# Performance work log

Measured on AMD Instinct MI355X. Metric: run time of the kernel, lower is better.

Reference implementation:

```python
import jax, jax.numpy as jnp
import numpy as np

BS, NCAMS, CIN, H, W = 4, 1, 256, 56, 200
MID = 128
DCH = 112  # (58-2)/0.5 depth bins
GX, GY, GZ = 128, 128, 16  # voxel grid


def setup_inputs() -> dict:
    key = jax.random.key(0)
    ks = jax.random.split(key, 32)
    f32 = jnp.float32

    def n(k, shape, scale=0.05):
        return jax.random.normal(k, shape, f32) * scale

    inp = {
        'img_feat': jax.random.normal(ks[0], (BS, NCAMS, CIN, H, W), f32),
        'scaled_pixel_size': jax.random.uniform(ks[1], (BS * NCAMS, 1), f32) * 2.0 + 0.5,
        # normalized sampling coords, slightly beyond [-1,1] to exercise zero padding
        'grids': jax.random.uniform(ks[2], (NCAMS, BS, GX, GY, GZ, 3), f32) * 2.2 - 1.1,
        # reduce_conv: Conv2d(CIN->MID,3x3,bias) + BN(affine, eval=per-channel scale/shift)
        'rc_w': n(ks[3], (MID, CIN, 3, 3)),
        'rc_b': n(ks[4], (MID,)),
        'rc_s': 1.0 + n(ks[5], (MID,)),
        'rc_t': n(ks[6], (MID,)),
        # Mlp(1 -> MID -> MID)
        'fc1_w': n(ks[7], (MID, 1), 0.5),
        'fc1_b': n(ks[8], (MID,)),
        'fc2_w': n(ks[9], (MID, MID)),
        'fc2_b': n(ks[10], (MID,)),
        # SELayer 1x1 convs (act on [N,MID,1,1] -> plain linears)
        'se_rw': n(ks[11], (MID, MID)),
        'se_rb': n(ks[12], (MID,)),
        'se_ew': n(ks[13], (MID, MID)),
        'se_eb': n(ks[14], (MID,)),
        # 3 BasicBlocks: conv3x3(no bias)+BN+ReLU+conv3x3(no bias)+BN, residual, ReLU
        'bb_w1': n(ks[15], (3, MID, MID, 3, 3)),
        'bb_s1': 1.0 + n(ks[16], (3, MID)),
        'bb_t1': n(ks[17], (3, MID)),
        'bb_w2': n(ks[18], (3, MID, MID, 3, 3)),
        'bb_s2': 1.0 + n(ks[19], (3, MID)),
        'bb_t2': n(ks[20], (3, MID)),
        # depth_pred 1x1 conv MID -> DCH
        'dp_w': n(ks[21], (DCH, MID)),
        'dp_b': n(ks[22], (DCH,)),
    }
    return inp


def _conv2d(x, w):
    return jax.lax.conv_general_dilated(x, w, (1, 1), 'SAME',
                                        dimension_numbers=('NCHW', 'OIHW', 'NCHW'))


def _aff(x, s, t):
    return x * s[None, :, None, None] + t[None, :, None, None]


def grid_sample_3d(feat, grid):
    """Trilinear grid_sample, zeros padding, align_corners=False.
    feat: [N,C,D,H,W]; grid: [N,X,Y,Z,3] with (x,y,z) in [-1,1] indexing (W,H,D).
    Returns [N,C,X,Y,Z]."""
    N, C, D, Hh, Ww = feat.shape
    ix = (grid[..., 0] + 1.0) * (Ww * 0.5) - 0.5
    iy = (grid[..., 1] + 1.0) * (Hh * 0.5) - 0.5
    iz = (grid[..., 2] + 1.0) * (D * 0.5) - 0.5
    x0 = jnp.floor(ix); y0 = jnp.floor(iy); z0 = jnp.floor(iz)
    fx, fy, fz = ix - x0, iy - y0, iz - z0

    def one(f, x0, y0, z0, fx, fy, fz):
        out = jnp.zeros((C,) + x0.shape, f.dtype)
        x0i = x0.astype(jnp.int32); y0i = y0.astype(jnp.int32); z0i = z0.astype(jnp.int32)
        for dz in (0, 1):
            for dy in (0, 1):
                for dx in (0, 1):
                    xi = x0i + dx; yi = y0i + dy; zi = z0i + dz
                    wgt = ((fx if dx else 1.0 - fx) * (fy if dy else 1.0 - fy)
                           * (fz if dz else 1.0 - fz))
                    valid = ((xi >= 0) & (xi < Ww) & (yi >= 0) & (yi < Hh)
                             & (zi >= 0) & (zi < D))
                    v = f[:, jnp.clip(zi, 0, D - 1), jnp.clip(yi, 0, Hh - 1),
                          jnp.clip(xi, 0, Ww - 1)]
                    out = out + v * (wgt * valid)[None]
        return out

    return jax.vmap(one)(feat, x0, y0, z0, fx, fy, fz)


def reference(img_feat, scaled_pixel_size, grids, rc_w, rc_b, rc_s, rc_t,
              fc1_w, fc1_b, fc2_w, fc2_b, se_rw, se_rb, se_ew, se_eb,
              bb_w1, bb_s1, bb_t1, bb_w2, bb_s2, bb_t2, dp_w, dp_b):
    bs, n_cams, c, h, w = img_feat.shape
    x = img_feat.reshape(bs * n_cams, c, h, w)
    # DepthNet (infer_mode): reduce_conv
    x = jax.nn.relu(_aff(_conv2d(x, rc_w) + rc_b[None, :, None, None], rc_s, rc_t))
    # Mlp on scaled_pixel_size + SE gating
    hmid = jax.nn.relu(scaled_pixel_size @ fc1_w.T + fc1_b) @ fc2_w.T + fc2_b
    se = jax.nn.relu(hmid @ se_rw.T + se_rb) @ se_ew.T + se_eb
    x = x * jax.nn.sigmoid(se)[:, :, None, None]
    # 3 BasicBlocks
    for i in range(3):
        y = jax.nn.relu(_aff(_conv2d(x, bb_w1[i]), bb_s1[i], bb_t1[i]))
        y = _aff(_conv2d(y, bb_w2[i]), bb_s2[i], bb_t2[i])
        x = jax.nn.relu(x + y)
    # depth_pred 1x1 conv, softmax over depth bins
    depth_feat = jnp.einsum('nchw,dc->ndhw', x, dp_w) + dp_b[None, :, None, None]
    depth = jax.nn.softmax(depth_feat, axis=1)
    depth = depth.reshape(bs, n_cams, 1, DCH, h, w)
    # per-camera frustum -> voxel bilinear sampling
    all_voxel_features = []
    for i in range(n_cams):
        all_voxel_features.append(grid_sample_3d(depth[:, i], grids[i]))
    agg = all_voxel_features[0]  # n_cams == 1 path in original forward
    return agg  # [bs, 1, GX, GY, GZ]
```

## Files before the change

### kernel.cpp

```cpp
#include <hip/hip_runtime.h>
#include <math.h>

typedef _Float16 v8h __attribute__((ext_vector_type(8)));
typedef float v4f __attribute__((ext_vector_type(4)));
typedef float v16f __attribute__((ext_vector_type(16)));

__global__ void __launch_bounds__(256) prep_kernel(
    const float* __restrict__ rc_w, const float* __restrict__ bb_w1,
    const float* __restrict__ bb_w2, const float* __restrict__ dp_w,
    const float* __restrict__ img, const float* __restrict__ sps,
    const float* __restrict__ fc1_w, const float* __restrict__ fc1_b,
    const float* __restrict__ fc2_w, const float* __restrict__ fc2_b,
    const float* __restrict__ se_rw, const float* __restrict__ se_rb,
    const float* __restrict__ se_ew, const float* __restrict__ se_eb,
    _Float16* __restrict__ wrc, _Float16* __restrict__ wbb,
    _Float16* __restrict__ wdp, _Float16* __restrict__ act16,
    float* __restrict__ sig) {
  const int bx = blockIdx.x;
  const int tid = threadIdx.x;
  __shared__ float lds[4612];

  if (bx < 64) {
    const float* src = rc_w + (size_t)bx * 2 * 2304;
#pragma unroll
    for (int r = 0; r < 18; ++r) {
      int e = r * 256 + tid;
      int col = e / 2304;
      int rem = e - col * 2304;
      lds[col * 2305 + rem] = src[e];
    }
    __syncthreads();
#pragma unroll
    for (int ro = 0; ro < 3; ++ro) {
      int lidx = ro * 256 + tid;
      if (lidx < 576) {
        int col = lidx & 1;
        int r = lidx >> 1;
        int kh = r & 1;
        int ct = r >> 1;
        int tap = ct % 9, c16 = ct / 9;
        v8h o;
#pragma unroll
        for (int j = 0; j < 8; ++j)
          o[j] = (_Float16)lds[col * 2305 + (c16 * 16 + kh * 8 + j) * 9 + tap];
        *(v8h*)(wrc + ((size_t)r * 128 + bx * 2 + col) * 8) = o;
      }
    }
  } else if (bx < 256) {
    const int t = bx - 64;
    const int k = t >> 5, g = t & 31;
    const float* base = (k < 3) ? (bb_w1 + (size_t)k * 147456)
                                : (bb_w2 + (size_t)(k - 3) * 147456);
    const int cslot = (k < 3) ? (2 * k) : (2 * (k - 3) + 1);
    const float* src = base + (size_t)g * 4 * 1152;
#pragma unroll
    for (int r = 0; r < 18; ++r) {
      int e = r * 256 + tid;
      int col = e / 1152;
      int rem = e - col * 1152;
      lds[col * 1153 + rem] = src[e];
    }
    __syncthreads();
#pragma unroll
    for (int ro = 0; ro < 3; ++ro) {
      int lidx = ro * 256 + tid;
      if (lidx < 576) {
        int col = lidx & 3;
        int r = lidx >> 2;
        int kh = r & 1;
        int ct = r >> 1;
        int tap = ct % 9, c16 = ct / 9;
        v8h o;
#pragma unroll
        for (int j = 0; j < 8; ++j)
          o[j] = (_Float16)lds[col * 1153 + (c16 * 16 + kh * 8 + j) * 9 + tap];
        *(v8h*)(wbb + (size_t)cslot * 147456 + ((size_t)r * 128 + g * 4 + col) * 8) = o;
      }
    }
  } else if (bx < 263) {
    int s3 = (bx - 256) * 256 + tid;
    v8h o;
#pragma unroll
    for (int j = 0; j < 8; ++j) o[j] = (_Float16)dp_w[(size_t)s3 * 8 + j];
    *(v8h*)(wdp + (size_t)s3 * 8) = o;
  } else if (bx < 267) {
    const int b = bx - 263;
    const int wv = tid >> 6, lane = tid & 63;
    const int row = wv * 32 + (lane >> 1);
    const int half = lane & 1;
    if (tid < 128) lds[tid] = fmaxf(sps[b] * fc1_w[tid] + fc1_b[tid], 0.f);
    __syncthreads();
    {
      const float4* wp = (const float4*)(fc2_w + (size_t)row * 128 + half * 64);
      float p = 0.f;
#pragma unroll
      for (int g = 0; g < 2; ++g) {
        float4 w[8];
#pragma unroll
        for (int m = 0; m < 8; ++m) w[m] = wp[g * 8 + m];
#pragma unroll
        for (int m = 0; m < 8; ++m) {
          const int k = half * 64 + g * 32 + m * 4;
          p += w[m].x * lds[k] + w[m].y * lds[k + 1] + w[m].z * lds[k + 2] +
               w[m].w * lds[k + 3];
        }
      }
      p += __shfl_xor(p, 1);
      if (half == 0) lds[128 + row] = p + fc2_b[row];
    }
    __syncthreads();
    {
      const float4* wp = (const float4*)(se_rw + (size_t)row * 128 + half * 64);
      float p = 0.f;
#pragma unroll
      for (int g = 0; g < 2; ++g) {
        float4 w[8];
#pragma unroll
        for (int m = 0; m < 8; ++m) w[m] = wp[g * 8 + m];
#pragma unroll
        for (int m = 0; m < 8; ++m) {
          const int k = 128 + half * 64 + g * 32 + m * 4;
          p += w[m].x * lds[k] + w[m].y * lds[k + 1] + w[m].z * lds[k + 2] +
               w[m].w * lds[k + 3];
        }
      }
      p += __shfl_xor(p, 1);
      if (half == 0) lds[256 + row] = fmaxf(p + se_rb[row], 0.f);
    }
    __syncthreads();
    {
      const float4* wp = (const float4*)(se_ew + (size_t)row * 128 + half * 64);
      float p = 0.f;
#pragma unroll
      for (int g = 0; g < 2; ++g) {
        float4 w[8];
#pragma unroll
        for (int m = 0; m < 8; ++m) w[m] = wp[g * 8 + m];
#pragma unroll
        for (int m = 0; m < 8; ++m) {
          const int k = 256 + half * 64 + g * 32 + m * 4;
          p += w[m].x * lds[k] + w[m].y * lds[k + 1] + w[m].z * lds[k + 2] +
               w[m].w * lds[k + 3];
        }
      }
      p += __shfl_xor(p, 1);
      if (half == 0) {
        float v = p + se_eb[row];
        sig[b * 128 + row] = 1.f / (1.f + expf(-v));
      }
    }
  } else {
    const int bid = bx - 267;
    const int cq = bid & 7;
    const int i = (bid >> 3) * 256 + tid;
    const int n = i / 11200;
    const int hw = i - n * 11200;
    const float* ip = img + (size_t)n * 2867200 + (size_t)(cq * 32) * 11200 + hw;
    float v[32];
#pragma unroll
    for (int k = 0; k < 32; ++k) v[k] = ip[(size_t)k * 11200];
    _Float16* op = act16 + (size_t)i * 256 + cq * 32;
#pragma unroll
    for (int g = 0; g < 4; ++g) {
      v8h o;
#pragma unroll
      for (int j = 0; j < 8; ++j) o[j] = (_Float16)v[g * 8 + j];
      *(v8h*)(op + g * 8) = o;
    }
  }
}

template <int CIN, int MODE>
__global__ void __launch_bounds__(512, 4) conv3x3_kernel(
    const _Float16* __restrict__ act, const _Float16* __restrict__ wr,
    const _Float16* __restrict__ xprev, const float* __restrict__ bias,
    const float* __restrict__ sc, const float* __restrict__ tr,
    const float* __restrict__ sig_se, _Float16* __restrict__ out) {
  constexpr int NCH = CIN / 16;
  const int wt = blockIdx.x, ht = blockIdx.y;
  const int n = blockIdx.z >> 1, cg = blockIdx.z & 1;
  const int h0 = ht * 8, w0 = wt * 32;
  const int tid = threadIdx.x;
  const int wave = tid >> 6, lane = tid & 63;
  const int l31 = lane & 31, khalf = lane >> 5;
  const int wv = wave >> 1, kc = wave & 1;

  __shared__ alignas(16) _Float16 ldsA[2][2 * 340 * 8];
  __shared__ alignas(16) _Float16 ldsB[2][1152 * 8];

  size_t goffA[2];
  int loffA[2];
  bool exA[2], okA[2];
#pragma unroll
  for (int it = 0; it < 2; ++it) {
    int slot = it * 512 + tid;
    int pos = slot >> 1, part = slot & 1;
    int hh = pos / 34, ww = pos - hh * 34;
    int gh = h0 - 1 + hh, gw = w0 - 1 + ww;
    exA[it] = slot < 680;
    bool inimg = (unsigned)gh < 56u && (unsigned)gw < 200u;
    okA[it] = exA[it] && inimg;
    loffA[it] = (part * 340 + pos) * 8;
    int ghc = okA[it] ? gh : 0, gwc = okA[it] ? gw : 0;
    goffA[it] = (((size_t)n * 56 + ghc) * 200 + gwc) * CIN + part * 8;
  }
  size_t goffB[3];
  int loffB[3];
  bool exB[3];
#pragma unroll
  for (int it = 0; it < 3; ++it) {
    int slot = it * 512 + tid;
    exB[it] = slot < 1152;
    int s = exB[it] ? slot : 0;
    int tap = s >> 7, kh = (s >> 6) & 1, co = s & 63;
    goffB[it] = (((size_t)(tap * 2 + kh)) * 128 + cg * 64 + co) * 8;
    loffB[it] = s * 8;
  }

  const v8h zero8 = {(_Float16)0, (_Float16)0, (_Float16)0, (_Float16)0,
                     (_Float16)0, (_Float16)0, (_Float16)0, (_Float16)0};
  v8h preA0[2], preB0[3], preA1[2], preB1[3];
#pragma unroll
  for (int it = 0; it < 2; ++it) {
    preA0[it] = okA[it] ? *(const v8h*)(act + goffA[it]) : zero8;
    preA1[it] = okA[it] ? *(const v8h*)(act + goffA[it] + 16) : zero8;
  }
#pragma unroll
  for (int it = 0; it < 3; ++it) {
    preB0[it] = exB[it] ? *(const v8h*)(wr + goffB[it]) : zero8;
    preB1[it] = exB[it] ? *(const v8h*)(wr + goffB[it] + 18432) : zero8;
  }

  v16f acc[2];
#pragma unroll
  for (int mt = 0; mt < 2; ++mt)
#pragma unroll
    for (int r = 0; r < 16; ++r) acc[mt][r] = 0.f;

  auto compute = [&](const _Float16* aB, const _Float16* bB) {
#pragma unroll
    for (int dx = 0; dx < 3; ++dx) {
      v8h a[4];
#pragma unroll
      for (int r = 0; r < 4; ++r)
        a[r] = *(const v8h*)(aB + (khalf * 340 + (wv * 2 + r) * 34 + l31 + dx) * 8);
#pragma unroll
      for (int dy = 0; dy < 3; ++dy) {
        v8h bf = *(const v8h*)(bB + ((dy * 3 + dx) * 128 + khalf * 64 + kc * 32 + l31) * 8);
        acc[0] = __builtin_amdgcn_mfma_f32_32x32x16_f16(a[dy], bf, acc[0], 0, 0, 0);
        acc[1] = __builtin_amdgcn_mfma_f32_32x32x16_f16(a[dy + 1], bf, acc[1], 0, 0, 0);
      }
    }
  };

#pragma unroll 1
  for (int c = 0; c < NCH; c += 2) {
#pragma unroll
    for (int it = 0; it < 2; ++it)
      if (exA[it]) *(v8h*)(&ldsA[0][0] + loffA[it]) = preA0[it];
#pragma unroll
    for (int it = 0; it < 3; ++it)
      if (exB[it]) *(v8h*)(&ldsB[0][0] + loffB[it]) = preB0[it];
    if (c + 2 < NCH) {
#pragma unroll
      for (int it = 0; it < 2; ++it)
        preA0[it] = okA[it] ? *(const v8h*)(act + goffA[it] + (size_t)(c + 2) * 16) : zero8;
#pragma unroll
      for (int it = 0; it < 3; ++it)
        preB0[it] = exB[it] ? *(const v8h*)(wr + goffB[it] + (size_t)(c + 2) * 18432) : zero8;
    }
    __syncthreads();
    compute(&ldsA[0][0], &ldsB[0][0]);

#pragma unroll
    for (int it = 0; it < 2; ++it)
      if (exA[it]) *(v8h*)(&ldsA[1][0] + loffA[it]) = preA1[it];
#pragma unroll
    for (int it = 0; it < 3; ++it)
      if (exB[it]) *(v8h*)(&ldsB[1][0] + loffB[it]) = preB1[it];
    if (c + 3 < NCH) {
#pragma unroll
      for (int it = 0; it < 2; ++it)
        preA1[it] = okA[it] ? *(const v8h*)(act + goffA[it] + (size_t)(c + 3) * 16) : zero8;
#pragma unroll
      for (int it = 0; it < 3; ++it)
        preB1[it] = exB[it] ? *(const v8h*)(wr + goffB[it] + (size_t)(c + 3) * 18432) : zero8;
    }
    __syncthreads();
    compute(&ldsA[1][0], &ldsB[1][0]);
  }

#pragma unroll
  for (int mt = 0; mt < 2; ++mt) {
    const int h = h0 + wv * 2 + mt;
    const int cc = cg * 64 + kc * 32 + l31;
    const float s = sc[cc], t = tr[cc];
    float bb = 0.f, sg = 1.f;
    if constexpr (MODE == 0) {
      bb = bias[cc];
      sg = sig_se[n * 128 + cc];
    }
#pragma unroll
    for (int r = 0; r < 16; ++r) {
      const int m = (r & 3) + 8 * (r >> 2) + 4 * khalf;
      const int w = w0 + m;
      if (w < 200) {
        float v = acc[mt][r];
        size_t oidx = (((size_t)n * 56 + h) * 200 + w) * 128 + cc;
        if constexpr (MODE == 0) v = fmaxf((v + bb) * s + t, 0.f) * sg;
        if constexpr (MODE == 1) v = fmaxf(v * s + t, 0.f);
        if constexpr (MODE == 2) v = fmaxf((float)xprev[oidx] + v * s + t, 0.f);
        out[oidx] = (_Float16)v;
      }
    }
  }
}

__global__ void __launch_bounds__(256) depth_proj_softmax_kernel(
    const _Float16* __restrict__ x, const _Float16* __restrict__ wdp,
    const float* __restrict__ dp_b, _Float16* __restrict__ depth) {
  const int wave = threadIdx.x >> 6, lane = threadIdx.x & 63;
  const int q = lane >> 4, l16 = lane & 15;
  const int pos0 = blockIdx.x * 64 + wave * 16;

  v4f acc[7];
#pragma unroll
  for (int nt = 0; nt < 7; ++nt) {
    float bv = dp_b[nt * 16 + l16];
    acc[nt] = {bv, bv, bv, bv};
  }
#pragma unroll
  for (int c0 = 0; c0 < 128; c0 += 32) {
    v8h a = *(const v8h*)(x + (size_t)(pos0 + l16) * 128 + c0 + q * 8);
#pragma unroll
    for (int nt = 0; nt < 7; ++nt) {
      v8h b = *(const v8h*)(wdp + (size_t)(nt * 16 + l16) * 128 + c0 + q * 8);
      acc[nt] = __builtin_amdgcn_mfma_f32_16x16x32_f16(a, b, acc[nt], 0, 0, 0);
    }
  }
  float m[4];
#pragma unroll
  for (int r = 0; r < 4; ++r) {
    m[r] = acc[0][r];
#pragma unroll
    for (int nt = 1; nt < 7; ++nt) m[r] = fmaxf(m[r], acc[nt][r]);
  }
#pragma unroll
  for (int off = 1; off < 16; off <<= 1)
#pragma unroll
    for (int r = 0; r < 4; ++r) m[r] = fmaxf(m[r], __shfl_xor(m[r], off));
  float s[4] = {0.f, 0.f, 0.f, 0.f};
#pragma unroll
  for (int nt = 0; nt < 7; ++nt)
#pragma unroll
    for (int r = 0; r < 4; ++r) {
      float e = expf(acc[nt][r] - m[r]);
      acc[nt][r] = e;
      s[r] += e;
    }
#pragma unroll
  for (int off = 1; off < 16; off <<= 1)
#pragma unroll
    for (int r = 0; r < 4; ++r) s[r] += __shfl_xor(s[r], off);
#pragma unroll
  for (int r = 0; r < 4; ++r) {
    const float inv = 1.f / s[r];
    const size_t p = pos0 + q * 4 + r;
#pragma unroll
    for (int nt = 0; nt < 7; ++nt)
      depth[p * 112 + nt * 16 + l16] = (_Float16)(acc[nt][r] * inv);
  }
}

__global__ void __launch_bounds__(256) gridsample_kernel(
    const float* __restrict__ grids, const _Float16* __restrict__ depth,
    float* __restrict__ out) {
  const int b = blockIdx.x;
  const int x = b & 7, s = b >> 3;
  const int i0 = (x >> 1) * 1024 + (x & 1) * 512 + s;
  const int i = i0 * 256 + (int)threadIdx.x;
  const int n = i >> 18;
  const float gx = grids[(size_t)i * 3];
  const float gy = grids[(size_t)i * 3 + 1];
  const float gz = grids[(size_t)i * 3 + 2];
  const float ix = (gx + 1.f) * 100.f - 0.5f;
  const float iy = (gy + 1.f) * 28.f - 0.5f;
  const float iz = (gz + 1.f) * 56.f - 0.5f;
  const float xf = floorf(ix), yf = floorf(iy), zf = floorf(iz);
  const int x0 = (int)xf, y0 = (int)yf, z0 = (int)zf;
  const float fx = ix - xf, fy = iy - yf, fz = iz - zf;
  const bool zv0 = (unsigned)z0 < 112u;
  const bool zv1 = (unsigned)(z0 + 1) < 112u;
  const float wz0 = 1.f - fz, wz1 = fz;
  float acc = 0.f;
#pragma unroll
  for (int dy = 0; dy < 2; ++dy) {
    const int yi = y0 + dy;
    const float wy = dy ? fy : 1.f - fy;
#pragma unroll
    for (int dx = 0; dx < 2; ++dx) {
      const int xi = x0 + dx;
      const float wx = dx ? fx : 1.f - fx;
      if ((unsigned)xi < 200u && (unsigned)yi < 56u) {
        const _Float16* bp = depth + ((size_t)n * 11200 + yi * 200 + xi) * 112;
        float v0 = zv0 ? (float)bp[z0] : 0.f;
        float v1 = zv1 ? (float)bp[z0 + 1] : 0.f;
        acc += (wx * wy) * (wz0 * v0 + wz1 * v1);
      }
    }
  }
  out[i] = acc;
}

extern "C" void kernel_launch(void* const* d_in, const int* in_sizes, int n_in,
                              void* d_out, int out_size, void* d_ws, size_t ws_size,
                              hipStream_t stream) {
  (void)in_sizes; (void)n_in; (void)out_size; (void)ws_size;
  const float* img = (const float*)d_in[0];
  const float* sps = (const float*)d_in[1];
  const float* grids = (const float*)d_in[2];
  const float* rc_w = (const float*)d_in[3];
  const float* rc_b = (const float*)d_in[4];
  const float* rc_s = (const float*)d_in[5];
  const float* rc_t = (const float*)d_in[6];
  const float* fc1_w = (const float*)d_in[7];
  const float* fc1_b = (const float*)d_in[8];
  const float* fc2_w = (const float*)d_in[9];
  const float* fc2_b = (const float*)d_in[10];
  const float* se_rw = (const float*)d_in[11];
  const float* se_rb = (const float*)d_in[12];
  const float* se_ew = (const float*)d_in[13];
  const float* se_eb = (const float*)d_in[14];
  const float* bb_w1 = (const float*)d_in[15];
  const float* bb_s1 = (const float*)d_in[16];
  const float* bb_t1 = (const float*)d_in[17];
  const float* bb_w2 = (const float*)d_in[18];
  const float* bb_s2 = (const float*)d_in[19];
  const float* bb_t2 = (const float*)d_in[20];
  const float* dp_w = (const float*)d_in[21];
  const float* dp_b = (const float*)d_in[22];
  float* outp = (float*)d_out;

  char* ws = (char*)d_ws;
  _Float16* act16 = (_Float16*)(ws + 0);
  _Float16* depth16 = (_Float16*)(ws + 0);
  _Float16* xa = (_Float16*)(ws + 23068672);
  _Float16* xb = (_Float16*)(ws + 23068672 + 11534336);
  _Float16* yb = (_Float16*)(ws + 23068672 + 2 * 11534336);
  _Float16* wrc = (_Float16*)(ws + 57671680);
  _Float16* wdp = (_Float16*)(ws + 57671680 + 589824);
  _Float16* wbb = (_Float16*)(ws + 58327040);
  float* sig = (float*)(ws + 58327040 + 1769472);

  prep_kernel<<<dim3(1667), 256, 0, stream>>>(
      rc_w, bb_w1, bb_w2, dp_w, img, sps, fc1_w, fc1_b, fc2_w, fc2_b, se_rw, se_rb,
      se_ew, se_eb, wrc, wbb, wdp, act16, sig);

  dim3 cgrid(7, 7, 8);
  conv3x3_kernel<256, 0><<<cgrid, 512, 0, stream>>>(act16, wrc, nullptr, rc_b, rc_s,
                                                    rc_t, sig, xa);
  _Float16* xcur = xa;
  _Float16* xnxt = xb;
  for (int i = 0; i < 3; ++i) {
    conv3x3_kernel<128, 1><<<cgrid, 512, 0, stream>>>(
        xcur, wbb + (size_t)(2 * i) * 147456, nullptr, nullptr, bb_s1 + i * 128,
        bb_t1 + i * 128, nullptr, yb);
    conv3x3_kernel<128, 2><<<cgrid, 512, 0, stream>>>(
        yb, wbb + (size_t)(2 * i + 1) * 147456, xcur, nullptr, bb_s2 + i * 128,
        bb_t2 + i * 128, nullptr, xnxt);
    _Float16* t = xcur;
    xcur = xnxt;
    xnxt = t;
  }

  depth_proj_softmax_kernel<<<dim3(700), 256, 0, stream>>>(xcur, wdp, dp_b, depth16);
  gridsample_kernel<<<dim3(4096), 256, 0, stream>>>(grids, depth16, outp);
}
```

Measured before the change: 401.1 us.

## Load conv weight tiles directly into LDS and use single-barrier double buffering

The implicit-GEMM conv kernel now copies its weight (B) tiles from global memory straight into LDS with the global_load_lds builtin. They no longer pass through registers and a separate LDS store. The main loop is restructured to process one channel chunk per iteration, with one barrier and one register prefetch for the activation tile. The weight copy for the next chunk goes into the alternate LDS buffer while the current chunk is computed. This reduces register pressure and VGPR-to-LDS store traffic. The risk is that the asynchronous LDS writes may not be fully ordered by the barrier, and the prefetch depth is halved.

```diff
diff --git a/kernel.cpp b/kernel.cpp
--- a/kernel.cpp
+++ b/kernel.cpp
@@ -4,6 +4,12 @@
 typedef _Float16 v8h __attribute__((ext_vector_type(8)));
 typedef float v4f __attribute__((ext_vector_type(4)));
 typedef float v16f __attribute__((ext_vector_type(16)));
+
+__device__ __forceinline__ void gload_lds16(const _Float16* g, _Float16* l) {
+  __builtin_amdgcn_global_load_lds(
+      (const __attribute__((address_space(1))) unsigned int*)(const void*)g,
+      (__attribute__((address_space(3))) unsigned int*)(void*)l, 16, 0, 0);
+}
 
 __global__ void __launch_bounds__(256) prep_kernel(
     const float* __restrict__ rc_w, const float* __restrict__ bb_w1,
@@ -205,7 +211,6 @@
     goffA[it] = (((size_t)n * 56 + ghc) * 200 + gwc) * CIN + part * 8;
   }
   size_t goffB[3];
-  int loffB[3];
   bool exB[3];
 #pragma unroll
   for (int it = 0; it < 3; ++it) {
@@ -214,22 +219,16 @@
     int s = exB[it] ? slot : 0;
     int tap = s >> 7, kh = (s >> 6) & 1, co = s & 63;
     goffB[it] = (((size_t)(tap * 2 + kh)) * 128 + cg * 64 + co) * 8;
-    loffB[it] = s * 8;
   }
 
   const v8h zero8 = {(_Float16)0, (_Float16)0, (_Float16)0, (_Float16)0,
                      (_Float16)0, (_Float16)0, (_Float16)0, (_Float16)0};
-  v8h preA0[2], preB0[3], preA1[2], preB1[3];
-#pragma unroll
-  for (int it = 0; it < 2; ++it) {
-    preA0[it] = okA[it] ? *(const v8h*)(act + goffA[it]) : zero8;
-    preA1[it] = okA[it] ? *(const v8h*)(act + goffA[it] + 16) : zero8;
-  }
-#pragma unroll
-  for (int it = 0; it < 3; ++it) {
-    preB0[it] = exB[it] ? *(const v8h*)(wr + goffB[it]) : zero8;
-    preB1[it] = exB[it] ? *(const v8h*)(wr + goffB[it] + 18432) : zero8;
-  }
+  v8h preA[2];
+#pragma unroll
+  for (int it = 0; it < 2; ++it) preA[it] = okA[it] ? *(const v8h*)(act + goffA[it]) : zero8;
+#pragma unroll
+  for (int it = 0; it < 3; ++it)
+    if (exB[it]) gload_lds16(wr + goffB[it], &ldsB[0][(it * 512 + tid) * 8]);
 
   v16f acc[2];
 #pragma unroll
@@ -237,7 +236,24 @@
 #pragma unroll
     for (int r = 0; r < 16; ++r) acc[mt][r] = 0.f;
 
-  auto compute = [&](const _Float16* aB, const _Float16* bB) {
+#pragma unroll 1
+  for (int c = 0; c < NCH; ++c) {
+    _Float16* aB = &ldsA[c & 1][0];
+#pragma unroll
+    for (int it = 0; it < 2; ++it)
+      if (exA[it]) *(v8h*)(aB + loffA[it]) = preA[it];
+    __syncthreads();
+    if (c + 1 < NCH) {
+#pragma unroll
+      for (int it = 0; it < 3; ++it)
+        if (exB[it])
+          gload_lds16(wr + goffB[it] + (size_t)(c + 1) * 18432,
+                      &ldsB[(c + 1) & 1][(it * 512 + tid) * 8]);
+#pragma unroll
+      for (int it = 0; it < 2; ++it)
+        preA[it] = okA[it] ? *(const v8h*)(act + goffA[it] + (size_t)(c + 1) * 16) : zero8;
+    }
+    const _Float16* bB = &ldsB[c & 1][0];
 #pragma unroll
     for (int dx = 0; dx < 3; ++dx) {
       v8h a[4];
@@ -251,43 +267,6 @@
         acc[1] = __builtin_amdgcn_mfma_f32_32x32x16_f16(a[dy + 1], bf, acc[1], 0, 0, 0);
       }
     }
-  };
-
-#pragma unroll 1
-  for (int c = 0; c < NCH; c += 2) {
-#pragma unroll
-    for (int it = 0; it < 2; ++it)
-      if (exA[it]) *(v8h*)(&ldsA[0][0] + loffA[it]) = preA0[it];
-#pragma unroll
-    for (int it = 0; it < 3; ++it)
-      if (exB[it]) *(v8h*)(&ldsB[0][0] + loffB[it]) = preB0[it];
-    if (c + 2 < NCH) {
-#pragma unroll
-      for (int it = 0; it < 2; ++it)
-        preA0[it] = okA[it] ? *(const v8h*)(act + goffA[it] + (size_t)(c + 2) * 16) : zero8;
-#pragma unroll
-      for (int it = 0; it < 3; ++it)
-        preB0[it] = exB[it] ? *(const v8h*)(wr + goffB[it] + (size_t)(c + 2) * 18432) : zero8;
-    }
-    __syncthreads();
-    compute(&ldsA[0][0], &ldsB[0][0]);
-
-#pragma unroll
-    for (int it = 0; it < 2; ++it)
-      if (exA[it]) *(v8h*)(&ldsA[1][0] + loffA[it]) = preA1[it];
-#pragma unroll
-    for (int it = 0; it < 3; ++it)
-      if (exB[it]) *(v8h*)(&ldsB[1][0] + loffB[it]) = preB1[it];
-    if (c + 3 < NCH) {
-#pragma unroll
-      for (int it = 0; it < 2; ++it)
-        preA1[it] = okA[it] ? *(const v8h*)(act + goffA[it] + (size_t)(c + 3) * 16) : zero8;
-#pragma unroll
-      for (int it = 0; it < 3; ++it)
-        preB1[it] = exB[it] ? *(const v8h*)(wr + goffB[it] + (size_t)(c + 3) * 18432) : zero8;
-    }
-    __syncthreads();
-    compute(&ldsA[1][0], &ldsB[1][0]);
   }
 
 #pragma unroll
```

After: 389.8 us. 1.03x faster.
